# Kernel tuning notes

Hardware: AMD Instinct MI355X
Metric: run time of the kernel (lower is better)

## Reference

```python
import jax, jax.numpy as jnp
import numpy as np


def _deform_conv2d(x, offset, weight, stride=(1, 1), pad=(1, 1), dilation=(1, 1)):
    # x: [B,C,H,W]; offset: [B, 2*Goff*kh*kw, oh, ow]; weight: [OC, C//Gw, kh, kw]
    B, C, H, W = x.shape
    OC, Cg, kh, kw = weight.shape
    Gw = C // Cg
    K = kh * kw
    sh, sw = stride
    ph, pw = pad
    dh, dw = dilation
    oh = (H + 2 * ph - (dh * (kh - 1) + 1)) // sh + 1
    ow = (W + 2 * pw - (dw * (kw - 1) + 1)) // sw + 1
    Goff = offset.shape[1] // (2 * K)
    # torchvision layout: per offset group, per kernel tap k, (dy, dx)
    off = offset.reshape(B, Goff, K, 2, oh, ow)
    ki = jnp.arange(K) // kw  # kernel row per tap
    kj = jnp.arange(K) % kw   # kernel col per tap
    base_y = jnp.arange(oh) * sh - ph
    base_x = jnp.arange(ow) * sw - pw
    gy = (base_y[None, :] + (ki * dh)[:, None]).astype(x.dtype)  # [K, oh]
    gx = (base_x[None, :] + (kj * dw)[:, None]).astype(x.dtype)  # [K, ow]
    py = off[:, :, :, 0] + gy[None, None, :, :, None]  # [B,Goff,K,oh,ow]
    px = off[:, :, :, 1] + gx[None, None, :, None, :]
    cpg = C // Goff  # channels per offset group
    py = jnp.repeat(py, cpg, axis=1)  # [B,C,K,oh,ow]
    px = jnp.repeat(px, cpg, axis=1)
    xf = x.reshape(B, C, H * W)
    y0 = jnp.floor(py)
    x0 = jnp.floor(px)
    ty = py - y0
    tx = px - x0
    y0i = y0.astype(jnp.int32)
    x0i = x0.astype(jnp.int32)

    def gather(cy, cx):
        valid = (cy >= 0) & (cy < H) & (cx >= 0) & (cx < W)
        idx = jnp.clip(cy, 0, H - 1) * W + jnp.clip(cx, 0, W - 1)
        v = jnp.take_along_axis(xf, idx.reshape(B, C, -1), axis=2).reshape(idx.shape)
        return jnp.where(valid, v, jnp.zeros((), x.dtype))

    # bilinear sample, zero padding outside image (matches torchvision)
    v = (gather(y0i, x0i) * (1 - ty) * (1 - tx)
         + gather(y0i, x0i + 1) * (1 - ty) * tx
         + gather(y0i + 1, x0i) * ty * (1 - tx)
         + gather(y0i + 1, x0i + 1) * ty * tx)  # [B,C,K,oh,ow]
    v = v.reshape(B, Gw, Cg, K, oh, ow)
    wg = weight.reshape(Gw, OC // Gw, Cg, K)
    out = jnp.einsum('bgckhw,gock->bgohw', v, wg)
    return out.reshape(B, OC, oh, ow)


def setup_inputs() -> dict:
    key = jax.random.key(0)
    k1, k2, k3 = jax.random.split(key, 3)
    x = jax.random.normal(k1, (8, 64, 56, 56), dtype=jnp.float32)
    offset = jax.random.normal(k2, (8, 18, 56, 56), dtype=jnp.float32)
    weight = jax.random.normal(k3, (64, 64, 3, 3), dtype=jnp.float32) * 0.05
    return {"input": x, "offset": offset, "weight": weight}


def reference(input, offset, weight):
    return _deform_conv2d(input, offset, weight, stride=(1, 1), pad=(1, 1), dilation=(1, 1))
```

## Files before the change

kernel.cpp:

```cpp
#include <hip/hip_runtime.h>
#include <hip/hip_fp16.h>


typedef _Float16 f16x8 __attribute__((ext_vector_type(8)));
typedef float    f32x4 __attribute__((ext_vector_type(4)));

namespace {
constexpr int Bn = 8, Cn = 64, Hn = 56, Wn = 56;
constexpr int Kk = 9, OCn = 64;
constexpr int NPIX = 56 * 56;
constexpr int CK   = Cn * Kk;
constexpr int TP   = 32;
constexpr int TILES = NPIX / TP;
constexpr int XTILES = NPIX / 64;
constexpr int KSTEPS = CK / 32;
}

__device__ __forceinline__ __half2 u2h(unsigned u) {
    union { unsigned u; __half2 h; } x; x.u = u; return x.h;
}
__device__ __forceinline__ unsigned bcast_h(float f) {
    unsigned short hs = __half_as_ushort(__float2half(f));
    return (unsigned)hs * 0x10001u;
}

__global__ __launch_bounds__(256) void prep_kernel(
    const float* __restrict__ x, const float* __restrict__ w,
    unsigned short* __restrict__ xh, unsigned short* __restrict__ wh2)
{
    const int tid = threadIdx.x;
    if (blockIdx.x >= 392) {
        const int i = (blockIdx.x - 392) * 256 + tid;
        if (i < OCn * CK) {
            const int j    = i & 7;
            const int lane = (i >> 3) & 63;
            const int rest = i >> 9;
            const int og   = rest / KSTEPS;
            const int oc   = og * 16 + (lane & 15);
            const int kglob = (rest % KSTEPS) * 32 + (lane >> 4) * 8 + j;
            const int tap = kglob >> 6;
            const int c   = kglob & 63;
            wh2[i] = __half_as_ushort(__float2half(w[oc * CK + c * Kk + tap]));
        }
        return;
    }
    __shared__ unsigned short lds[64][66];
    const int b  = blockIdx.x / XTILES;
    const int t0 = (blockIdx.x % XTILES) * 64;
    const float* xb = x + (size_t)b * Cn * NPIX;
    {
        const int hw0 = (tid & 15) * 4;
        #pragma unroll
        for (int i = 0; i < 4; ++i) {
            const int c = (tid >> 4) + i * 16;
            const float4 v = *(const float4*)(xb + (size_t)c * NPIX + t0 + hw0);
            lds[hw0 + 0][c] = __half_as_ushort(__float2half(v.x));
            lds[hw0 + 1][c] = __half_as_ushort(__float2half(v.y));
            lds[hw0 + 2][c] = __half_as_ushort(__float2half(v.z));
            lds[hw0 + 3][c] = __half_as_ushort(__float2half(v.w));
        }
    }
    __syncthreads();
    {
        const int co = (tid & 7) * 8;
        #pragma unroll
        for (int i = 0; i < 2; ++i) {
            const int hw = (tid >> 3) + i * 32;
            unsigned short tmp[8] __attribute__((aligned(16)));
            #pragma unroll
            for (int j = 0; j < 8; ++j) tmp[j] = lds[hw][co + j];
            *(uint4*)(xh + ((size_t)b * NPIX + t0 + hw) * Cn + co) = *(const uint4*)tmp;
        }
    }
}

__global__ __launch_bounds__(256, 4) void deform_fused(
    const unsigned short* __restrict__ xh, const float* __restrict__ off,
    const unsigned short* __restrict__ wh2, float* __restrict__ out)
{
    __shared__ uint4 smpw[Kk * TP];
    __shared__ int4  smpa[Kk * TP];
    __shared__ __align__(16) uint4 vbuf[3][8 * TP];

    const int tid = threadIdx.x;
    const int b  = blockIdx.x / TILES;
    const int p0 = (blockIdx.x % TILES) * TP;
    const unsigned short* xb = xh + (size_t)b * NPIX * Cn;
    const float* offb = off + (size_t)b * 18 * NPIX;

    for (int e = tid; e < Kk * TP; e += 256) {
        const int k  = e >> 5;
        const int px = e & 31;
        const int p  = p0 + px;
        const int oy = p / Wn, ox = p % Wn;
        const int ki = k / 3, kj = k % 3;
        const float offy = offb[(size_t)(2 * k)     * NPIX + p];
        const float offx = offb[(size_t)(2 * k + 1) * NPIX + p];
        const float py  = offy + (float)(oy - 1 + ki);
        const float pxv = offx + (float)(ox - 1 + kj);
        const float y0f = floorf(py), x0f = floorf(pxv);
        const float ty = py - y0f, tx = pxv - x0f;
        const int y0 = (int)y0f, x0 = (int)x0f;
        const int y1 = y0 + 1, x1 = x0 + 1;
        const bool vy0 = (y0 >= 0) & (y0 < Hn);
        const bool vy1 = (y1 >= 0) & (y1 < Hn);
        const bool vx0 = (x0 >= 0) & (x0 < Wn);
        const bool vx1 = (x1 >= 0) & (x1 < Wn);
        const int cy0 = min(max(y0, 0), Hn - 1);
        const int cy1 = min(max(y1, 0), Hn - 1);
        const int cx0 = min(max(x0, 0), Wn - 1);
        const int cx1 = min(max(x1, 0), Wn - 1);
        uint4 wq;
        wq.x = bcast_h((vy0 && vx0) ? (1.f - ty) * (1.f - tx) : 0.f);
        wq.y = bcast_h((vy0 && vx1) ? (1.f - ty) * tx         : 0.f);
        wq.z = bcast_h((vy1 && vx0) ? ty * (1.f - tx)         : 0.f);
        wq.w = bcast_h((vy1 && vx1) ? ty * tx                 : 0.f);
        int4 av;
        av.x = (cy0 * Wn + cx0) * Cn;
        av.y = (cy0 * Wn + cx1) * Cn;
        av.z = (cy1 * Wn + cx0) * Cn;
        av.w = (cy1 * Wn + cx1) * Cn;
        smpw[e] = wq;
        smpa[e] = av;
    }
    __syncthreads();

    const int oct = tid & 7;
    const int gpx = (tid >> 3) & 31;
    const int co  = oct * 8;

    const int lane = tid & 63;
    const int og   = tid >> 6;
    const int hi   = lane >> 4;
    const int lr   = lane & 15;
    const uint4* ab = (const uint4*)wh2 + (size_t)og * KSTEPS * 64 + lane;

    uint4 s0[3], s1[3], s2[3], s3[3], wqr[3];
    uint4 aF[2][2];
    f32x4 acc0 = {0.f, 0.f, 0.f, 0.f};
    f32x4 acc1 = {0.f, 0.f, 0.f, 0.f};

    auto stage = [&](int k) {
        const int sl = k % 3;
        const int m  = k * TP + gpx;
        const int4 av = smpa[m];
        wqr[sl] = smpw[m];
        s0[sl] = *(const uint4*)(xb + av.x + co);
        s1[sl] = *(const uint4*)(xb + av.y + co);
        s2[sl] = *(const uint4*)(xb + av.z + co);
        s3[sl] = *(const uint4*)(xb + av.w + co);
    };
    auto loadA = [&](int k) {
        const int sl = k & 1;
        aF[sl][0] = ab[(k * 2 + 0) * 64];
        aF[sl][1] = ab[(k * 2 + 1) * 64];
    };
    auto blend = [&](int k) {
        const int sl = k % 3;
        const __half2 w00 = u2h(wqr[sl].x), w01 = u2h(wqr[sl].y);
        const __half2 w10 = u2h(wqr[sl].z), w11 = u2h(wqr[sl].w);
        uint4 res;
        unsigned* rp = (unsigned*)&res;
        #pragma unroll
        for (int q = 0; q < 4; ++q) {
            __half2 a = __hmul2(w00, u2h(((const unsigned*)&s0[sl])[q]));
            a = __hfma2(w01, u2h(((const unsigned*)&s1[sl])[q]), a);
            a = __hfma2(w10, u2h(((const unsigned*)&s2[sl])[q]), a);
            a = __hfma2(w11, u2h(((const unsigned*)&s3[sl])[q]), a);
            rp[q] = *(const unsigned*)&a;
        }
        vbuf[sl][oct * TP + gpx] = res;
    };
    auto mfma = [&](int k) {
        const int sl = k % 3;
        #pragma unroll
        for (int kl = 0; kl < 2; ++kl) {
            const int octr = kl * 4 + hi;
            union { uint4 u; f16x8 h; } a, b0, b1;
            a.u  = aF[k & 1][kl];
            b0.u = vbuf[sl][octr * TP + lr];
            b1.u = vbuf[sl][octr * TP + 16 + lr];
            acc0 = __builtin_amdgcn_mfma_f32_16x16x32_f16(a.h, b0.h, acc0, 0, 0, 0);
            acc1 = __builtin_amdgcn_mfma_f32_16x16x32_f16(a.h, b1.h, acc1, 0, 0, 0);
        }
    };

    stage(0); stage(1); stage(2);
    loadA(0);
    blend(0);
    __syncthreads();

    #pragma unroll
    for (int k = 0; k < Kk; ++k) {
        if (k < Kk - 3) stage(k + 3);
        if (k < Kk - 1) loadA(k + 1);
        if (k < Kk - 1) blend(k + 1);
        mfma(k);
        __syncthreads();
    }

    float* ob = out + ((size_t)b * OCn + og * 16 + hi * 4) * NPIX + p0 + lr;
    #pragma unroll
    for (int r = 0; r < 4; ++r) {
        ob[(size_t)r * NPIX]      = acc0[r];
        ob[(size_t)r * NPIX + 16] = acc1[r];
    }
}

extern "C" void kernel_launch(void* const* d_in, const int* in_sizes, int n_in,
                              void* d_out, int out_size, void* d_ws, size_t ws_size,
                              hipStream_t stream) {
    const float* x   = (const float*)d_in[0];
    const float* off = (const float*)d_in[1];
    const float* w   = (const float*)d_in[2];
    float* out = (float*)d_out;
    unsigned short* wh2 = (unsigned short*)d_ws;
    unsigned short* xh  = (unsigned short*)((char*)d_ws + 131072);

    hipLaunchKernelGGL(prep_kernel, dim3(392 + 144), dim3(256), 0, stream, x, w, xh, wh2);
    hipLaunchKernelGGL(deform_fused, dim3(Bn * TILES), dim3(256), 0, stream,
                       xh, off, wh2, out);
}
```

Baseline: 21.96 us.

## Restructure deform conv into single-wave blocks with register-resident bilinear blending

The fused kernel changes from 256-thread blocks covering 32 pixels, which used LDS for sample metadata and blended values plus a barrier per tap, to 64-thread single-wave blocks covering 16 pixels. Each lane now computes its own sampling metadata, gathers and blends directly into the MFMA B-operand layout in registers, and issues MFMAs for all four output-channel groups. This removes the LDS round trips and __syncthreads. In exchange each wave reloads the full weight matrix, metadata computation is repeated across the lanes that share a pixel, and the grid gets twice as many smaller blocks.

```diff
diff --git a/kernel.cpp b/kernel.cpp
--- a/kernel.cpp
+++ b/kernel.cpp
@@ -10,10 +10,10 @@
 constexpr int Kk = 9, OCn = 64;
 constexpr int NPIX = 56 * 56;
 constexpr int CK   = Cn * Kk;
-constexpr int TP   = 32;
-constexpr int TILES = NPIX / TP;
+constexpr int KSTEPS = CK / 32;
+constexpr int TPW  = 16;
+constexpr int TILES = NPIX / TPW;
 constexpr int XTILES = NPIX / 64;
-constexpr int KSTEPS = CK / 32;
 }
 
 __device__ __forceinline__ __half2 u2h(unsigned u) {
@@ -74,30 +74,38 @@
     }
 }
 
-__global__ __launch_bounds__(256, 4) void deform_fused(
+__global__ __launch_bounds__(64, 2) void deform_fused(
     const unsigned short* __restrict__ xh, const float* __restrict__ off,
     const unsigned short* __restrict__ wh2, float* __restrict__ out)
 {
-    __shared__ uint4 smpw[Kk * TP];
-    __shared__ int4  smpa[Kk * TP];
-    __shared__ __align__(16) uint4 vbuf[3][8 * TP];
-
-    const int tid = threadIdx.x;
+    const int lane = threadIdx.x;
+    const int lr   = lane & 15;
+    const int hi   = lane >> 4;
     const int b  = blockIdx.x / TILES;
-    const int p0 = (blockIdx.x % TILES) * TP;
+    const int p0 = (blockIdx.x % TILES) * TPW;
+    const int p  = p0 + lr;
+    const int oy = p / Wn, ox = p % Wn;
+
     const unsigned short* xb = xh + (size_t)b * NPIX * Cn;
-    const float* offb = off + (size_t)b * 18 * NPIX;
-
-    for (int e = tid; e < Kk * TP; e += 256) {
-        const int k  = e >> 5;
-        const int px = e & 31;
-        const int p  = p0 + px;
-        const int oy = p / Wn, ox = p % Wn;
-        const int ki = k / 3, kj = k % 3;
-        const float offy = offb[(size_t)(2 * k)     * NPIX + p];
-        const float offx = offb[(size_t)(2 * k + 1) * NPIX + p];
-        const float py  = offy + (float)(oy - 1 + ki);
-        const float pxv = offx + (float)(ox - 1 + kj);
+    const float* offp = off + (size_t)b * 18 * NPIX + p;
+    const uint4* ab = (const uint4*)wh2 + lane;
+
+    float offv[18];
+    #pragma unroll
+    for (int t = 0; t < 18; ++t) offv[t] = offp[(size_t)t * NPIX];
+
+    unsigned wqs[2][4];
+    int4     avs[2];
+    uint4 aF[2][4];
+    uint4 s0[3], s1[3], s2[3], s3[3];
+    f32x4 acc[4] = {{0.f,0.f,0.f,0.f},{0.f,0.f,0.f,0.f},
+                    {0.f,0.f,0.f,0.f},{0.f,0.f,0.f,0.f}};
+
+    auto meta = [&](int t) {
+        const int sl = t & 1;
+        const int ki = t / 3, kj = t % 3;
+        const float py  = offv[2*t]   + (float)(oy - 1 + ki);
+        const float pxv = offv[2*t+1] + (float)(ox - 1 + kj);
         const float y0f = floorf(py), x0f = floorf(pxv);
         const float ty = py - y0f, tx = pxv - x0f;
         const int y0 = (int)y0f, x0 = (int)x0f;
@@ -110,100 +118,71 @@
         const int cy1 = min(max(y1, 0), Hn - 1);
         const int cx0 = min(max(x0, 0), Wn - 1);
         const int cx1 = min(max(x1, 0), Wn - 1);
-        uint4 wq;
-        wq.x = bcast_h((vy0 && vx0) ? (1.f - ty) * (1.f - tx) : 0.f);
-        wq.y = bcast_h((vy0 && vx1) ? (1.f - ty) * tx         : 0.f);
-        wq.z = bcast_h((vy1 && vx0) ? ty * (1.f - tx)         : 0.f);
-        wq.w = bcast_h((vy1 && vx1) ? ty * tx                 : 0.f);
-        int4 av;
-        av.x = (cy0 * Wn + cx0) * Cn;
-        av.y = (cy0 * Wn + cx1) * Cn;
-        av.z = (cy1 * Wn + cx0) * Cn;
-        av.w = (cy1 * Wn + cx1) * Cn;
-        smpw[e] = wq;
-        smpa[e] = av;
-    }
-    __syncthreads();
-
-    const int oct = tid & 7;
-    const int gpx = (tid >> 3) & 31;
-    const int co  = oct * 8;
-
-    const int lane = tid & 63;
-    const int og   = tid >> 6;
-    const int hi   = lane >> 4;
-    const int lr   = lane & 15;
-    const uint4* ab = (const uint4*)wh2 + (size_t)og * KSTEPS * 64 + lane;
-
-    uint4 s0[3], s1[3], s2[3], s3[3], wqr[3];
-    uint4 aF[2][2];
-    f32x4 acc0 = {0.f, 0.f, 0.f, 0.f};
-    f32x4 acc1 = {0.f, 0.f, 0.f, 0.f};
-
-    auto stage = [&](int k) {
-        const int sl = k % 3;
-        const int m  = k * TP + gpx;
-        const int4 av = smpa[m];
-        wqr[sl] = smpw[m];
+        wqs[sl][0] = bcast_h((vy0 && vx0) ? (1.f - ty) * (1.f - tx) : 0.f);
+        wqs[sl][1] = bcast_h((vy0 && vx1) ? (1.f - ty) * tx         : 0.f);
+        wqs[sl][2] = bcast_h((vy1 && vx0) ? ty * (1.f - tx)         : 0.f);
+        wqs[sl][3] = bcast_h((vy1 && vx1) ? ty * tx                 : 0.f);
+        avs[sl].x = (cy0 * Wn + cx0) * Cn;
+        avs[sl].y = (cy0 * Wn + cx1) * Cn;
+        avs[sl].z = (cy1 * Wn + cx0) * Cn;
+        avs[sl].w = (cy1 * Wn + cx1) * Cn;
+    };
+    auto stage = [&](int ks) {
+        const int sl = ks % 3;
+        const int4 av = avs[(ks >> 1) & 1];
+        const int co = (hi + (ks & 1) * 4) * 8;
         s0[sl] = *(const uint4*)(xb + av.x + co);
         s1[sl] = *(const uint4*)(xb + av.y + co);
         s2[sl] = *(const uint4*)(xb + av.z + co);
         s3[sl] = *(const uint4*)(xb + av.w + co);
     };
-    auto loadA = [&](int k) {
-        const int sl = k & 1;
-        aF[sl][0] = ab[(k * 2 + 0) * 64];
-        aF[sl][1] = ab[(k * 2 + 1) * 64];
+    auto loadA = [&](int ks) {
+        const int sl = ks & 1;
+        #pragma unroll
+        for (int og = 0; og < 4; ++og)
+            aF[sl][og] = ab[(og * KSTEPS + ks) * 64];
     };
-    auto blend = [&](int k) {
-        const int sl = k % 3;
-        const __half2 w00 = u2h(wqr[sl].x), w01 = u2h(wqr[sl].y);
-        const __half2 w10 = u2h(wqr[sl].z), w11 = u2h(wqr[sl].w);
-        uint4 res;
-        unsigned* rp = (unsigned*)&res;
+
+    loadA(0);
+    meta(0);
+    stage(0);
+    stage(1);
+    meta(1);
+    stage(2);
+
+    #pragma unroll
+    for (int ks = 0; ks < KSTEPS; ++ks) {
+        const int sl = ks % 3;
+        const unsigned* wq = wqs[(ks >> 1) & 1];
+        const __half2 w00 = u2h(wq[0]), w01 = u2h(wq[1]);
+        const __half2 w10 = u2h(wq[2]), w11 = u2h(wq[3]);
+        union { unsigned u[4]; f16x8 h; } bf;
         #pragma unroll
         for (int q = 0; q < 4; ++q) {
             __half2 a = __hmul2(w00, u2h(((const unsigned*)&s0[sl])[q]));
             a = __hfma2(w01, u2h(((const unsigned*)&s1[sl])[q]), a);
             a = __hfma2(w10, u2h(((const unsigned*)&s2[sl])[q]), a);
             a = __hfma2(w11, u2h(((const unsigned*)&s3[sl])[q]), a);
-            rp[q] = *(const unsigned*)&a;
-        }
-        vbuf[sl][oct * TP + gpx] = res;
-    };
-    auto mfma = [&](int k) {
-        const int sl = k % 3;
-        #pragma unroll
-        for (int kl = 0; kl < 2; ++kl) {
-            const int octr = kl * 4 + hi;
-            union { uint4 u; f16x8 h; } a, b0, b1;
-            a.u  = aF[k & 1][kl];
-            b0.u = vbuf[sl][octr * TP + lr];
-            b1.u = vbuf[sl][octr * TP + 16 + lr];
-            acc0 = __builtin_amdgcn_mfma_f32_16x16x32_f16(a.h, b0.h, acc0, 0, 0, 0);
-            acc1 = __builtin_amdgcn_mfma_f32_16x16x32_f16(a.h, b1.h, acc1, 0, 0, 0);
-        }
-    };
-
-    stage(0); stage(1); stage(2);
-    loadA(0);
-    blend(0);
-    __syncthreads();
+            bf.u[q] = *(const unsigned*)&a;
+        }
+        if (ks + 3 < KSTEPS) {
+            if (((ks + 3) & 1) == 0) meta((ks + 3) >> 1);
+            stage(ks + 3);
+        }
+        if (ks + 1 < KSTEPS) loadA(ks + 1);
+        #pragma unroll
+        for (int og = 0; og < 4; ++og) {
+            union { uint4 u; f16x8 h; } a;
+            a.u = aF[ks & 1][og];
+            acc[og] = __builtin_amdgcn_mfma_f32_16x16x32_f16(a.h, bf.h, acc[og], 0, 0, 0);
+        }
+    }
 
     #pragma unroll
-    for (int k = 0; k < Kk; ++k) {
-        if (k < Kk - 3) stage(k + 3);
-        if (k < Kk - 1) loadA(k + 1);
-        if (k < Kk - 1) blend(k + 1);
-        mfma(k);
-        __syncthreads();
-    }
-
-    float* ob = out + ((size_t)b * OCn + og * 16 + hi * 4) * NPIX + p0 + lr;
-    #pragma unroll
-    for (int r = 0; r < 4; ++r) {
-        ob[(size_t)r * NPIX]      = acc0[r];
-        ob[(size_t)r * NPIX + 16] = acc1[r];
+    for (int og = 0; og < 4; ++og) {
+        float* ob = out + ((size_t)b * OCn + og * 16 + hi * 4) * NPIX + p0 + lr;
+        #pragma unroll
+        for (int r = 0; r < 4; ++r) ob[(size_t)r * NPIX] = acc[og][r];
     }
 }
 
@@ -218,6 +197,6 @@
     unsigned short* xh  = (unsigned short*)((char*)d_ws + 131072);
 
     hipLaunchKernelGGL(prep_kernel, dim3(392 + 144), dim3(256), 0, stream, x, w, xh, wh2);
-    hipLaunchKernelGGL(deform_fused, dim3(Bn * TILES), dim3(256), 0, stream,
+    hipLaunchKernelGGL(deform_fused, dim3(Bn * TILES), dim3(64), 0, stream,
                        xh, off, wh2, out);
 }
```

Result: slower. 31.43 us (+43.1%).
